# Optimization experiments

Measured on AMD Instinct MI355X. Metric: run time of the kernel, lower is better.

## Reference

```python
import jax, jax.numpy as jnp
import numpy as np

B = 32          # number of graphs/segments
N_PER = 1024    # nodes per graph (equal segments)
N = B * N_PER
DIM = 3
SIGMA = 0.2


def setup_inputs() -> dict:
    key = jax.random.key(0)
    k1, k2, k3, k4 = jax.random.split(key, 4)
    src_pos = jax.random.normal(k1, (N, DIM), dtype=jnp.float32)
    tgt_pos = jax.random.normal(k2, (N, DIM), dtype=jnp.float32)
    # equal-sized contiguous segments: 0,0,...,1,1,...,B-1
    src_batch = jnp.repeat(jnp.arange(B, dtype=jnp.int64), N_PER)
    tgt_batch = jnp.repeat(jnp.arange(B, dtype=jnp.int64), N_PER)
    W = jax.random.normal(k3, (1, 2), dtype=jnp.float32) * 0.5
    b = jnp.zeros((1,), dtype=jnp.float32)
    return {"src_pos": src_pos, "tgt_pos": tgt_pos,
            "src_batch": src_batch, "tgt_batch": tgt_batch,
            "W": W, "b": b}


def _segment_mean(x, seg, num_segments):
    s = jax.ops.segment_sum(x, seg, num_segments=num_segments)
    cnt = jax.ops.segment_sum(jnp.ones((x.shape[0], 1), x.dtype), seg,
                              num_segments=num_segments)
    return s / cnt


def _weight_head(pos, seg, W, b):
    # SE(3)-invariant features: squared radius from per-graph centroid + bias feature
    cent = _segment_mean(pos, seg, B)                  # [B,3]
    centered = pos - cent[seg]                          # [N,3]
    r_sq = jnp.sum(centered * centered, axis=1, keepdims=True)  # [N,1]
    feat = jnp.concatenate([r_sq, jnp.ones_like(r_sq)], axis=1)  # [N,2]
    w = jax.nn.sigmoid(feat @ W.T + b).squeeze(-1)      # [N]
    return w + 1e-4


def _gauss_kernel(x, y, sigma):
    # x:[B,n,3], y:[B,m,3] -> K:[B,n,m]
    sq = (jnp.sum(x * x, -1)[:, :, None] + jnp.sum(y * y, -1)[:, None, :]
          - 2.0 * jnp.einsum('bnd,bmd->bnm', x, y))
    return jnp.exp(-sq / (2.0 * sigma * sigma))


def _kde_mmd(src_pos, tgt_pos, src_seg, tgt_seg, w_src, w_tgt, sigma):
    # center=True: subtract per-graph centroid
    src_c = src_pos - _segment_mean(src_pos, src_seg, B)[src_seg]
    tgt_c = tgt_pos - _segment_mean(tgt_pos, tgt_seg, B)[tgt_seg]
    # equal-sized segments -> block-diagonal pairwise structure via reshape
    x = src_c.reshape(B, N_PER, DIM)
    y = tgt_c.reshape(B, N_PER, DIM)
    wx = w_src.reshape(B, N_PER)
    wy = w_tgt.reshape(B, N_PER)
    # normalize weights per segment (KDE mixture weights)
    wx = wx / jnp.sum(wx, axis=1, keepdims=True)
    wy = wy / jnp.sum(wy, axis=1, keepdims=True)
    kxx = _gauss_kernel(x, x, sigma)
    kyy = _gauss_kernel(y, y, sigma)
    kxy = _gauss_kernel(x, y, sigma)
    txx = jnp.einsum('bn,bnm,bm->b', wx, kxx, wx)
    tyy = jnp.einsum('bn,bnm,bm->b', wy, kyy, wy)
    txy = jnp.einsum('bn,bnm,bm->b', wx, kxy, wy)
    per_graph = txx + tyy - 2.0 * txy                   # [B]
    return jnp.mean(per_graph)


def reference(src_pos, tgt_pos, src_batch, tgt_batch, W, b):
    w_src = _weight_head(src_pos, src_batch, W, b)
    w_tgt = _weight_head(tgt_pos, tgt_batch, W, b)
    loss = _kde_mmd(src_pos, tgt_pos, src_batch, tgt_batch, w_src, w_tgt, SIGMA)
    return loss
```

## Files before the change

kernel.cpp:

```cpp
#include <hip/hip_runtime.h>

#define BGR 32
#define N_PER 1024
#define NEGC (-18.033688011112043f)

__device__ __forceinline__ float fast_exp2(float x) {
#if __has_builtin(__builtin_amdgcn_exp2f)
    return __builtin_amdgcn_exp2f(x);
#else
    return exp2f(x);
#endif
}


__global__ __launch_bounds__(256) void prep_kernel(
    const float* __restrict__ src_pos, const float* __restrict__ tgt_pos,
    const float* __restrict__ W, const float* __restrict__ bias,
    float4* __restrict__ colbuf, float* __restrict__ wsum)
{
    const int blk  = blockIdx.x;
    const int side = blk >> 5;
    const int b    = blk & 31;
    const float* pos = (side ? tgt_pos : src_pos) + (size_t)b * N_PER * 3;
    const int t = threadIdx.x;
    const int lane = t & 63, wv = t >> 6;

    const float4* p4 = (const float4*)pos;
    float4 p0 = p4[3*t + 0];
    float4 p1 = p4[3*t + 1];
    float4 p2 = p4[3*t + 2];
    float nx[4] = {p0.x, p0.w, p1.z, p2.y};
    float ny[4] = {p0.y, p1.x, p1.w, p2.z};
    float nz[4] = {p0.z, p1.y, p2.x, p2.w};

    float sx = nx[0]+nx[1]+nx[2]+nx[3];
    float sy = ny[0]+ny[1]+ny[2]+ny[3];
    float sz = nz[0]+nz[1]+nz[2]+nz[3];
    #pragma unroll
    for (int off = 32; off; off >>= 1) {
        sx += __shfl_down(sx, off);
        sy += __shfl_down(sy, off);
        sz += __shfl_down(sz, off);
    }
    __shared__ float shred[12];
    __shared__ float cent[3];
    if (lane == 0) { shred[wv*3+0] = sx; shred[wv*3+1] = sy; shred[wv*3+2] = sz; }
    __syncthreads();
    if (t == 0) {
        float cx = 0.f, cy = 0.f, cz = 0.f;
        #pragma unroll
        for (int i = 0; i < 4; i++) { cx += shred[i*3]; cy += shred[i*3+1]; cz += shred[i*3+2]; }
        cent[0] = cx * (1.f/N_PER); cent[1] = cy * (1.f/N_PER); cent[2] = cz * (1.f/N_PER);
    }
    __syncthreads();
    const float cx = cent[0], cy = cent[1], cz = cent[2];
    const float w0 = W[0], w1 = W[1], bb = bias[0];

    float4 outv[4];
    float lwsum = 0.f;
    #pragma unroll
    for (int i = 0; i < 4; i++) {
        float x = nx[i] - cx, y = ny[i] - cy, z = nz[i] - cz;
        float rsq = x*x + y*y + z*z;
        float logit = rsq * w0 + w1 + bb;
        float w = 1.f / (1.f + __expf(-logit)) + 1e-4f;
        lwsum += w;
        outv[i] = make_float4(x, y, z, w);
    }
    float4* outp = colbuf + ((size_t)(side*BGR + b)) * N_PER + t*4;
    outp[0] = outv[0]; outp[1] = outv[1]; outp[2] = outv[2]; outp[3] = outv[3];

    #pragma unroll
    for (int off = 32; off; off >>= 1) lwsum += __shfl_down(lwsum, off);
    __shared__ float shw[4];
    if (lane == 0) shw[wv] = lwsum;
    __syncthreads();
    if (t == 0) wsum[side*BGR + b] = shw[0] + shw[1] + shw[2] + shw[3];
}

__global__ __launch_bounds__(256) void pair_kernel(
    const float4* __restrict__ colbuf, float* __restrict__ T)
{
    const int tile = blockIdx.x;
    const int b    = blockIdx.y;
    const int kind = blockIdx.z;
    const int rowside = (kind == 1) ? 1 : 0;
    const int colside = (kind == 0) ? 0 : 1;
    const float4* rows = colbuf + ((size_t)(rowside*BGR + b)) * N_PER;
    const float4* cols = colbuf + ((size_t)(colside*BGR + b)) * N_PER;

    __shared__ float4 lds[N_PER];
    const int t = threadIdx.x;
    #pragma unroll
    for (int i = 0; i < 4; i++) lds[t + 256*i] = cols[t + 256*i];
    __syncthreads();

    const int lane = t & 63, q = t >> 6;
    const int r0 = tile*128 + lane;
    const float4 ra = rows[r0];
    const float4 rb = rows[r0 + 64];
    float acca = 0.f, accb = 0.f;
    const int m0 = q * 256;
    #pragma unroll 4
    for (int m = m0; m < m0 + 256; ++m) {
        float4 c = lds[m];
        float dxa = ra.x - c.x, dya = ra.y - c.y, dza = ra.z - c.z;
        float dxb = rb.x - c.x, dyb = rb.y - c.y, dzb = rb.z - c.z;
        float da = dxa*dxa + dya*dya + dza*dza;
        float db = dxb*dxb + dyb*dyb + dzb*dzb;
        float ka = fast_exp2(da * NEGC);
        float kb = fast_exp2(db * NEGC);
        acca = fmaf(ka, c.w, acca);
        accb = fmaf(kb, c.w, accb);
    }
    float acc = acca * ra.w + accb * rb.w;
    #pragma unroll
    for (int off = 32; off; off >>= 1) acc += __shfl_down(acc, off);
    __shared__ float sh[4];
    if (lane == 0) sh[q] = acc;
    __syncthreads();
    if (t == 0) atomicAdd(&T[kind*BGR + b], sh[0] + sh[1] + sh[2] + sh[3]);
}

__global__ __launch_bounds__(64) void final_kernel(
    const float* __restrict__ T, const float* __restrict__ wsum,
    float* __restrict__ out)
{
    const int t = threadIdx.x;
    float v = 0.f;
    if (t < BGR) {
        float Sx = wsum[t], Sy = wsum[BGR + t];
        float txx = T[t] / (Sx * Sx);
        float tyy = T[BGR + t] / (Sy * Sy);
        float txy = T[2*BGR + t] / (Sx * Sy);
        v = txx + tyy - 2.f * txy;
    }
    #pragma unroll
    for (int off = 32; off; off >>= 1) v += __shfl_down(v, off);
    if (t == 0) out[0] = v * (1.f / BGR);
}

extern "C" void kernel_launch(void* const* d_in, const int* in_sizes, int n_in,
                              void* d_out, int out_size, void* d_ws, size_t ws_size,
                              hipStream_t stream) {
    const float* src_pos = (const float*)d_in[0];
    const float* tgt_pos = (const float*)d_in[1];
    const float* W    = (const float*)d_in[4];
    const float* bias = (const float*)d_in[5];

    float4* colbuf = (float4*)d_ws;
    float*  wsum   = (float*)((char*)d_ws + (size_t)2 * BGR * N_PER * sizeof(float4));
    float*  T      = wsum + 2*BGR;

    hipMemsetAsync(T, 0, 3*BGR*sizeof(float), stream);
    prep_kernel<<<64, 256, 0, stream>>>(src_pos, tgt_pos, W, bias, colbuf, wsum);
    pair_kernel<<<dim3(8, BGR, 3), 256, 0, stream>>>(colbuf, T);
    final_kernel<<<1, 64, 0, stream>>>(T, wsum, (float*)d_out);
}
```

Baseline: 97.21 us.

## Fold weights and norms into exponent; fuse final reduction via last-block counter

Each node now stores log2(weight) plus its scaled squared norm, so every pair reduces to three FMAs and one exp2 with no weight multiply. The memset and final kernel are removed: prep zeroes the accumulators and a counter, and the last pair block computes the loss. This trims ALU work in the hot loop and two launches, but exp2 of large combined terms may lose precision or overflow for distant points. The inner loop is also unrolled further.

```diff
diff --git a/kernel.cpp b/kernel.cpp
--- a/kernel.cpp
+++ b/kernel.cpp
@@ -3,6 +3,8 @@
 #define BGR 32
 #define N_PER 1024
 #define NEGC (-18.033688011112043f)
+#define SCAL (36.067376022224086f)
+#define NBLK (8 * BGR * 3)
 
 __device__ __forceinline__ float fast_exp2(float x) {
 #if __has_builtin(__builtin_amdgcn_exp2f)
@@ -16,7 +18,8 @@
 __global__ __launch_bounds__(256) void prep_kernel(
     const float* __restrict__ src_pos, const float* __restrict__ tgt_pos,
     const float* __restrict__ W, const float* __restrict__ bias,
-    float4* __restrict__ colbuf, float* __restrict__ wsum)
+    float4* __restrict__ nodebuf, float* __restrict__ wsum,
+    float* __restrict__ T, int* __restrict__ counter)
 {
     const int blk  = blockIdx.x;
     const int side = blk >> 5;
@@ -54,7 +57,7 @@
     }
     __syncthreads();
     const float cx = cent[0], cy = cent[1], cz = cent[2];
-    const float w0 = W[0], w1 = W[1], bb = bias[0];
+    const float w0 = W[0], w1b = W[1] + bias[0];
 
     float4 outv[4];
     float lwsum = 0.f;
@@ -62,12 +65,13 @@
     for (int i = 0; i < 4; i++) {
         float x = nx[i] - cx, y = ny[i] - cy, z = nz[i] - cz;
         float rsq = x*x + y*y + z*z;
-        float logit = rsq * w0 + w1 + bb;
+        float logit = rsq * w0 + w1b;
         float w = 1.f / (1.f + __expf(-logit)) + 1e-4f;
         lwsum += w;
-        outv[i] = make_float4(x, y, z, w);
+        float A = fmaf(NEGC, rsq, __log2f(w));
+        outv[i] = make_float4(x, y, z, A);
     }
-    float4* outp = colbuf + ((size_t)(side*BGR + b)) * N_PER + t*4;
+    float4* outp = nodebuf + ((size_t)(side*BGR + b)) * N_PER + t*4;
     outp[0] = outv[0]; outp[1] = outv[1]; outp[2] = outv[2]; outp[3] = outv[3];
 
     #pragma unroll
@@ -76,18 +80,24 @@
     if (lane == 0) shw[wv] = lwsum;
     __syncthreads();
     if (t == 0) wsum[side*BGR + b] = shw[0] + shw[1] + shw[2] + shw[3];
+
+    if (blk == 0) {
+        if (t < 3*BGR) T[t] = 0.f;
+        if (t == 0) *counter = 0;
+    }
 }
 
 __global__ __launch_bounds__(256) void pair_kernel(
-    const float4* __restrict__ colbuf, float* __restrict__ T)
+    const float4* __restrict__ nodebuf, const float* __restrict__ wsum,
+    float* __restrict__ T, int* __restrict__ counter, float* __restrict__ out)
 {
     const int tile = blockIdx.x;
     const int b    = blockIdx.y;
     const int kind = blockIdx.z;
     const int rowside = (kind == 1) ? 1 : 0;
     const int colside = (kind == 0) ? 0 : 1;
-    const float4* rows = colbuf + ((size_t)(rowside*BGR + b)) * N_PER;
-    const float4* cols = colbuf + ((size_t)(colside*BGR + b)) * N_PER;
+    const float4* rows = nodebuf + ((size_t)(rowside*BGR + b)) * N_PER;
+    const float4* cols = nodebuf + ((size_t)(colside*BGR + b)) * N_PER;
 
     __shared__ float4 lds[N_PER];
     const int t = threadIdx.x;
@@ -99,45 +109,52 @@
     const int r0 = tile*128 + lane;
     const float4 ra = rows[r0];
     const float4 rb = rows[r0 + 64];
+    const float rax = SCAL*ra.x, ray = SCAL*ra.y, raz = SCAL*ra.z, raA = ra.w;
+    const float rbx = SCAL*rb.x, rby = SCAL*rb.y, rbz = SCAL*rb.z, rbA = rb.w;
     float acca = 0.f, accb = 0.f;
     const int m0 = q * 256;
-    #pragma unroll 4
+    #pragma unroll 8
     for (int m = m0; m < m0 + 256; ++m) {
         float4 c = lds[m];
-        float dxa = ra.x - c.x, dya = ra.y - c.y, dza = ra.z - c.z;
-        float dxb = rb.x - c.x, dyb = rb.y - c.y, dzb = rb.z - c.z;
-        float da = dxa*dxa + dya*dya + dza*dza;
-        float db = dxb*dxb + dyb*dyb + dzb*dzb;
-        float ka = fast_exp2(da * NEGC);
-        float kb = fast_exp2(db * NEGC);
-        acca = fmaf(ka, c.w, acca);
-        accb = fmaf(kb, c.w, accb);
+        float ta = fmaf(rax, c.x, c.w + raA);
+        ta = fmaf(ray, c.y, ta);
+        ta = fmaf(raz, c.z, ta);
+        acca += fast_exp2(ta);
+        float tb = fmaf(rbx, c.x, c.w + rbA);
+        tb = fmaf(rby, c.y, tb);
+        tb = fmaf(rbz, c.z, tb);
+        accb += fast_exp2(tb);
     }
-    float acc = acca * ra.w + accb * rb.w;
+    float acc = acca + accb;
     #pragma unroll
     for (int off = 32; off; off >>= 1) acc += __shfl_down(acc, off);
     __shared__ float sh[4];
+    __shared__ int islast;
     if (lane == 0) sh[q] = acc;
     __syncthreads();
-    if (t == 0) atomicAdd(&T[kind*BGR + b], sh[0] + sh[1] + sh[2] + sh[3]);
-}
-
-__global__ __launch_bounds__(64) void final_kernel(
-    const float* __restrict__ T, const float* __restrict__ wsum,
-    float* __restrict__ out)
-{
-    const int t = threadIdx.x;
-    float v = 0.f;
-    if (t < BGR) {
-        float Sx = wsum[t], Sy = wsum[BGR + t];
-        float txx = T[t] / (Sx * Sx);
-        float tyy = T[BGR + t] / (Sy * Sy);
-        float txy = T[2*BGR + t] / (Sx * Sy);
-        v = txx + tyy - 2.f * txy;
+    if (t == 0) {
+        atomicAdd(&T[kind*BGR + b], sh[0] + sh[1] + sh[2] + sh[3]);
+        __threadfence();
+        int old = __hip_atomic_fetch_add(counter, 1, __ATOMIC_ACQ_REL,
+                                         __HIP_MEMORY_SCOPE_AGENT);
+        islast = (old == NBLK - 1);
     }
-    #pragma unroll
-    for (int off = 32; off; off >>= 1) v += __shfl_down(v, off);
-    if (t == 0) out[0] = v * (1.f / BGR);
+    __syncthreads();
+    if (islast) {
+        float v = 0.f;
+        if (t < BGR) {
+            float Sx = wsum[t], Sy = wsum[BGR + t];
+            float txx = __hip_atomic_load(&T[t],        __ATOMIC_RELAXED, __HIP_MEMORY_SCOPE_AGENT);
+            float tyy = __hip_atomic_load(&T[BGR + t],  __ATOMIC_RELAXED, __HIP_MEMORY_SCOPE_AGENT);
+            float txy = __hip_atomic_load(&T[2*BGR + t],__ATOMIC_RELAXED, __HIP_MEMORY_SCOPE_AGENT);
+            v = txx / (Sx * Sx) + tyy / (Sy * Sy) - 2.f * txy / (Sx * Sy);
+        }
+        if (t < 64) {
+            #pragma unroll
+            for (int off = 32; off; off >>= 1) v += __shfl_down(v, off);
+            if (t == 0) out[0] = v * (1.f / BGR);
+        }
+    }
 }
 
 extern "C" void kernel_launch(void* const* d_in, const int* in_sizes, int n_in,
@@ -148,12 +165,13 @@
     const float* W    = (const float*)d_in[4];
     const float* bias = (const float*)d_in[5];
 
-    float4* colbuf = (float4*)d_ws;
-    float*  wsum   = (float*)((char*)d_ws + (size_t)2 * BGR * N_PER * sizeof(float4));
-    float*  T      = wsum + 2*BGR;
+    float4* nodebuf = (float4*)d_ws;
+    float*  wsum    = (float*)((char*)d_ws + (size_t)2 * BGR * N_PER * sizeof(float4));
+    float*  T       = (float*)((char*)d_ws + (size_t)2 * BGR * N_PER * sizeof(float4) + 256);
+    int*    counter = (int*)  ((char*)d_ws + (size_t)2 * BGR * N_PER * sizeof(float4) + 1024);
 
-    hipMemsetAsync(T, 0, 3*BGR*sizeof(float), stream);
-    prep_kernel<<<64, 256, 0, stream>>>(src_pos, tgt_pos, W, bias, colbuf, wsum);
-    pair_kernel<<<dim3(8, BGR, 3), 256, 0, stream>>>(colbuf, T);
-    final_kernel<<<1, 64, 0, stream>>>(T, wsum, (float*)d_out);
+    prep_kernel<<<64, 256, 0, stream>>>(src_pos, tgt_pos, W, bias,
+                                        nodebuf, wsum, T, counter);
+    pair_kernel<<<dim3(8, BGR, 3), 256, 0, stream>>>(nodebuf, wsum, T, counter,
+                                                     (float*)d_out);
 }
```

Measured after the change: 99.28 us. 2.1% more time.
